# Kernel tuning notes

Hardware: AMD Instinct MI355X
Metric: run time of the kernel (lower is better)

Reference implementation:

```python
import jax, jax.numpy as jnp
import numpy as np

B, S, V, E, H = 256, 256, 32000, 1024, 1024


def setup_inputs() -> dict:
    key = jax.random.key(0)
    k0, k1, k2, k3 = jax.random.split(key, 4)
    inputs = jax.random.randint(k0, (B, S), 0, V, dtype=jnp.int32)
    emb = jax.random.normal(k1, (V, E), dtype=jnp.float32) * 0.02
    # Combined gate weights in flax LSTMCell gate order (i, f, g, o).
    # flax uses per-gate Dense layers; stacking them into [E,4H]/[H,4H] is equivalent.
    Wi = jax.random.normal(k2, (E, 4 * H), dtype=jnp.float32) * 0.02  # input->gates (no bias in flax dense_i)
    Wh = jax.random.normal(k3, (H, 4 * H), dtype=jnp.float32) * 0.02  # hidden->gates
    b = jnp.zeros((4 * H,), dtype=jnp.float32)  # bias lives on dense_h in flax
    return {"inputs": inputs, "emb": emb, "Wi": Wi, "Wh": Wh, "b": b}


def reference(inputs, emb, Wi, Wh, b):
    x = emb[inputs]  # [B,S,E] embedding lookup
    # Precompute all input projections at once (math-identical, one big GEMM).
    xW = jnp.einsum('bse,eg->bsg', x, Wi) + b  # [B,S,4H]

    def step(carry, xw_t):
        h, c = carry
        z = xw_t + h @ Wh  # [B,4H]
        i, f, g, o = jnp.split(z, 4, axis=-1)
        c = jax.nn.sigmoid(f) * c + jax.nn.sigmoid(i) * jnp.tanh(g)
        h = jax.nn.sigmoid(o) * jnp.tanh(c)
        return (h, c), h

    h0 = jnp.zeros((x.shape[0], Wh.shape[0]), dtype=x.dtype)
    (h, c), outs = jax.lax.scan(step, (h0, h0), jnp.swapaxes(xW, 0, 1))  # scan over time
    outputs = jnp.swapaxes(outs, 0, 1)  # [B,S,H]
    return outputs, h, c
```

## Files before the change

### kernel.cpp

```cpp
#include <hip/hip_runtime.h>
#include <hip/hip_bf16.h>
#include <stdint.h>


#define B_ 256
#define S_ 256
#define E_ 1024
#define H_ 1024
#define G_ 4096
#define M_ 65536

typedef float  f32x4  __attribute__((ext_vector_type(4)));
typedef __bf16 bf16x8 __attribute__((ext_vector_type(8)));

#define MFMA16(a, b, c) __builtin_amdgcn_mfma_f32_16x16x32_bf16((a), (b), (c), 0, 0, 0)

__device__ __forceinline__ void gload_lds16(const void* g, void* l) {
  __builtin_amdgcn_global_load_lds(
      (__attribute__((address_space(1))) void*)(g),
      (__attribute__((address_space(3))) void*)(l), 16, 0, 0);
}

__device__ __forceinline__ float sigm(float x) { return 1.f / (1.f + __expf(-x)); }
__device__ __forceinline__ float tanhfast(float x) {
  float e = __expf(-2.f * x);
  return (1.f - e) / (1.f + e);
}
__device__ __forceinline__ float bf_lo(unsigned v) { return __uint_as_float(v << 16); }
__device__ __forceinline__ float bf_hi(unsigned v) { return __uint_as_float(v & 0xffff0000u); }

__global__ __launch_bounds__(256) void zero_init(uint4* h16) {
  int i = blockIdx.x * 256 + threadIdx.x;
  uint4 z; z.x = z.y = z.z = z.w = 0u;
  if (i < 32768) h16[i] = z;
}
__global__ __launch_bounds__(256) void zero_flags(unsigned* flags) {
  flags[blockIdx.x * 256 + threadIdx.x] = 0u;
}

__global__ __launch_bounds__(256) void transpose_cast(const float* __restrict__ in,
                                                      __bf16* __restrict__ out) {
  __shared__ __bf16 tile[32][33];
  const int c0 = blockIdx.x * 32;
  const int r0 = blockIdx.y * 32;
  const int tx = threadIdx.x & 31, ty = threadIdx.x >> 5;
#pragma unroll
  for (int p = 0; p < 4; ++p) {
    const int rr = ty + p * 8;
    tile[rr][tx] = (__bf16)in[(size_t)(r0 + rr) * G_ + c0 + tx];
  }
  __syncthreads();
#pragma unroll
  for (int p = 0; p < 4; ++p) {
    const int rr = ty + p * 8;
    out[(size_t)(c0 + rr) * E_ + r0 + tx] = tile[tx][rr];
  }
}

union U16b { uint4 v; __bf16 h[8]; };
__global__ __launch_bounds__(256) void gather_cast(const int* __restrict__ idx,
                                                   const float* __restrict__ emb,
                                                   __bf16* __restrict__ X) {
  const size_t gid  = (size_t)blockIdx.x * 256 + threadIdx.x;
  const size_t base = gid * 8;
  const int r = (int)(base >> 10);
  const int e = (int)(base & 1023);
  const int row = idx[r];
  const float4* s = (const float4*)(emb + (size_t)row * E_ + e);
  const float4 v0 = s[0], v1 = s[1];
  U16b u;
  u.h[0] = (__bf16)v0.x; u.h[1] = (__bf16)v0.y; u.h[2] = (__bf16)v0.z; u.h[3] = (__bf16)v0.w;
  u.h[4] = (__bf16)v1.x; u.h[5] = (__bf16)v1.y; u.h[6] = (__bf16)v1.z; u.h[7] = (__bf16)v1.w;
  *(uint4*)(X + base) = u.v;
}

__global__ __launch_bounds__(256) void gemm_xw(const __bf16* __restrict__ X,
                                               const __bf16* __restrict__ WiT,
                                               const float* __restrict__ bias,
                                               __bf16* __restrict__ XW2) {
  __shared__ __bf16 As[128 * 32];
  __shared__ __bf16 Bs[128 * 32];
  __shared__ __bf16 eps[64][136];
  const int tid = threadIdx.x;
  const int lane = tid & 63;
  const int wid = tid >> 6;
  const int bn = blockIdx.x & 31;
  const int bm = blockIdx.x >> 5;
  const int row0 = bm * 128, col0 = bn * 128;
  const int wr = (wid >> 1) * 64, wc = (wid & 1) * 64;
  const int srow = tid >> 2, schunk = tid & 3;
  const char* gA = (const char*)(X + (size_t)(row0 + srow) * E_) + schunk * 16;
  const char* gB = (const char*)(WiT + (size_t)(col0 + srow) * E_) + schunk * 16;
  char* lA = (char*)As + wid * 1024;
  char* lB = (char*)Bs + wid * 1024;
  const int fr = lane & 15, kb = lane >> 4;

  f32x4 acc[4][4] = {};

  for (int kt = 0; kt < 32; ++kt) {
    gload_lds16(gA + kt * 64,              lA);
    gload_lds16(gA + kt * 64 + 64 * 2048,  lA + 4096);
    gload_lds16(gB + kt * 64,              lB);
    gload_lds16(gB + kt * 64 + 64 * 2048,  lB + 4096);
    __syncthreads();
    bf16x8 a[4], b[4];
#pragma unroll
    for (int m = 0; m < 4; ++m)
      a[m] = *(const bf16x8*)((const char*)As + (wr + m * 16 + fr) * 64 + kb * 16);
#pragma unroll
    for (int n = 0; n < 4; ++n)
      b[n] = *(const bf16x8*)((const char*)Bs + (wc + n * 16 + fr) * 64 + kb * 16);
#pragma unroll
    for (int m = 0; m < 4; ++m)
#pragma unroll
      for (int n = 0; n < 4; ++n)
        acc[m][n] = MFMA16(a[m], b[n], acc[m][n]);
    __syncthreads();
  }

  float bv[4];
#pragma unroll
  for (int n = 0; n < 4; ++n) bv[n] = bias[col0 + wc + n * 16 + fr];

  const int gate = col0 >> 10;
  const int cg0  = (col0 & 1023) >> 5;

#pragma unroll
  for (int h = 0; h < 2; ++h) {
    if ((wid >> 1) == h) {
#pragma unroll
      for (int m = 0; m < 4; ++m)
#pragma unroll
        for (int n = 0; n < 4; ++n)
#pragma unroll
          for (int r = 0; r < 4; ++r)
            eps[m * 16 + kb * 4 + r][wc + n * 16 + fr] = (__bf16)(acc[m][n][r] + bv[n]);
    }
    __syncthreads();
    {
      const int row = tid >> 2, ch = tid & 3;
      const int r_m = row0 + h * 64 + row;
      const uint4* s = (const uint4*)&eps[row][ch * 32];
      uint4* d = (uint4*)(XW2 + ((size_t)r_m * 32 + (cg0 + ch)) * 128 + gate * 32);
#pragma unroll
      for (int i = 0; i < 4; ++i) d[i] = s[i];
    }
    __syncthreads();
  }
}

__global__ __launch_bounds__(512, 2) void lstm_scan(
    const __bf16* __restrict__ WhT, const __bf16* __restrict__ XW2,
    __bf16* __restrict__ hb0, __bf16* __restrict__ hb1,
    float* __restrict__ outp, float* __restrict__ hfin,
    float* __restrict__ cfin, unsigned* __restrict__ flags) {
  __shared__ __bf16 As[32 * 1024];
  __shared__ float  zs[4][32][34];
  __shared__ int    sgrp[2];
  const int tid = threadIdx.x;
  const int lane = tid & 63;
  const int wid = tid >> 6;

  if (tid == 0) {
    unsigned xcd;
    asm volatile("s_getreg_b32 %0, hwreg(HW_REG_XCC_ID)" : "=s"(xcd));
    xcd &= 7u;
    unsigned slot = __hip_atomic_fetch_add(&flags[512 + xcd], 1u,
                                           __ATOMIC_RELAXED, __HIP_MEMORY_SCOPE_AGENT);
    sgrp[0] = (int)xcd;
    sgrp[1] = (int)(slot & 31u);
  }
  __syncthreads();
  const int bg = sgrp[0];
  const int cg = sgrp[1];
  const int b0 = bg * 32;
  const int c0 = cg * 32;
  unsigned* grpflags = flags + bg * 64;

  const int wg = wid & 3;
  const int nh = wid >> 2;
  const int fr = lane & 15, kb = lane >> 4;
  const __bf16* wb = WhT + (size_t)(wg * 1024 + c0 + nh * 16 + fr) * H_ + kb * 8;

  bf16x8 W[32];
#pragma unroll
  for (int j = 0; j < 32; ++j) W[j] = *(const bf16x8*)(wb + j * 32);

  const int crow = tid >> 4, ccolb = (tid & 15) * 2;
  const size_t sidx = (size_t)(b0 + crow) * H_ + c0 + ccolb;
  const __bf16* xwrow = XW2 + ((size_t)(b0 + crow) * S_ * 32 + cg) * 128 + ccolb;
  float creg0 = 0.f, creg1 = 0.f;

#pragma unroll 1
  for (int t = 0; t < S_; ++t) {
    const __bf16* hin = (t & 1) ? hb1 : hb0;
    __bf16* hout = (t & 1) ? hb0 : hb1;

    const __bf16* p = xwrow + (size_t)t * 4096;
    const unsigned xw0 = *(const unsigned*)(p);
    const unsigned xw1 = *(const unsigned*)(p + 32);
    const unsigned xw2 = *(const unsigned*)(p + 64);
    const unsigned xw3 = *(const unsigned*)(p + 96);

    if (t > 0) {
      if (tid < 32) {
        const unsigned tgt = (unsigned)t;
        while (__hip_atomic_load(&grpflags[tid], __ATOMIC_RELAXED,
                                 __HIP_MEMORY_SCOPE_AGENT) < tgt)
          __builtin_amdgcn_s_sleep(1);
      }
      __syncthreads();
    }

    {
      uint4 sv[8];
#pragma unroll
      for (int i = 0; i < 8; ++i) {
        const int ci = i * 512 + tid;
        const int row = ci >> 7, cch = ci & 127;
        const void* src = (const char*)(hin + (size_t)(b0 + row) * H_) + cch * 16;
        asm volatile("global_load_dwordx4 %0, %1, off sc0"
                     : "=&v"(sv[i]) : "v"(src) : "memory");
      }
      asm volatile("s_waitcnt vmcnt(0)" ::: "memory");
      __builtin_amdgcn_sched_barrier(0);
#pragma unroll
      for (int i = 0; i < 8; ++i) {
        const int ci = i * 512 + tid;
        const int row = ci >> 7, cch = ci & 127;
        *(uint4*)((char*)As + row * 2048 + ((cch ^ (row & 7)) * 16)) = sv[i];
      }
    }
    __syncthreads();

    f32x4 acc0 = {0.f, 0.f, 0.f, 0.f}, acc1 = {0.f, 0.f, 0.f, 0.f};
#pragma unroll
    for (int j = 0; j < 32; ++j) {
      const int ck = j * 4 + kb;
      bf16x8 alo = *(const bf16x8*)((const char*)As + fr * 2048 +
                                    ((ck ^ (fr & 7)) * 16));
      bf16x8 ahi = *(const bf16x8*)((const char*)As + (16 + fr) * 2048 +
                                    ((ck ^ (fr & 7)) * 16));
      acc0 = MFMA16(alo, W[j], acc0);
      acc1 = MFMA16(ahi, W[j], acc1);
    }
#pragma unroll
    for (int r = 0; r < 4; ++r) {
      zs[wg][kb * 4 + r][nh * 16 + fr]      = acc0[r];
      zs[wg][16 + kb * 4 + r][nh * 16 + fr] = acc1[r];
    }
    __syncthreads();

    const float2 zi2 = *(const float2*)&zs[0][crow][ccolb];
    const float2 zf2 = *(const float2*)&zs[1][crow][ccolb];
    const float2 zg2 = *(const float2*)&zs[2][crow][ccolb];
    const float2 zo2 = *(const float2*)&zs[3][crow][ccolb];
    const float zi0 = zi2.x + bf_lo(xw0), zi1 = zi2.y + bf_hi(xw0);
    const float zf0 = zf2.x + bf_lo(xw1), zf1 = zf2.y + bf_hi(xw1);
    const float zg0 = zg2.x + bf_lo(xw2), zg1 = zg2.y + bf_hi(xw2);
    const float zo0 = zo2.x + bf_lo(xw3), zo1 = zo2.y + bf_hi(xw3);
    const float cv0 = sigm(zf0) * creg0 + sigm(zi0) * tanhfast(zg0);
    const float cv1 = sigm(zf1) * creg1 + sigm(zi1) * tanhfast(zg1);
    creg0 = cv0; creg1 = cv1;
    const float hv0 = sigm(zo0) * tanhfast(cv0);
    const float hv1 = sigm(zo1) * tanhfast(cv1);

    union { __bf16 h[2]; unsigned u; } up;
    up.h[0] = (__bf16)hv0; up.h[1] = (__bf16)hv1;
    float2 o2; o2.x = hv0; o2.y = hv1;

    {
      void* dst = (void*)(hout + sidx);
      asm volatile("global_store_dword %0, %1, off sc0"
                   :: "v"(dst), "v"(up.u) : "memory");
    }

    if (t == S_ - 1) {
      *(float2*)(outp + ((size_t)(b0 + crow) * S_ + t) * H_ + c0 + ccolb) = o2;
      float2 c2; c2.x = cv0; c2.y = cv1;
      *(float2*)(hfin + sidx) = o2;
      *(float2*)(cfin + sidx) = c2;
    } else {
      asm volatile("s_waitcnt vmcnt(0)" ::: "memory");
      __builtin_amdgcn_s_barrier();
      if (tid == 0)
        __hip_atomic_store(&grpflags[cg], (unsigned)(t + 1),
                           __ATOMIC_RELAXED, __HIP_MEMORY_SCOPE_AGENT);
      *(float2*)(outp + ((size_t)(b0 + crow) * S_ + t) * H_ + c0 + ccolb) = o2;
    }
  }
}

extern "C" void kernel_launch(void* const* d_in, const int* in_sizes, int n_in,
                              void* d_out, int out_size, void* d_ws, size_t ws_size,
                              hipStream_t stream) {
  const int*   inp  = (const int*)d_in[0];
  const float* emb  = (const float*)d_in[1];
  const float* Wi   = (const float*)d_in[2];
  const float* Wh   = (const float*)d_in[3];
  const float* bias = (const float*)d_in[4];

  char* ws = (char*)d_ws;
  __bf16* WiT = (__bf16*)(ws);
  __bf16* WhT = (__bf16*)(ws + 8388608);
  __bf16* hb0 = (__bf16*)(ws + 16777216);
  __bf16* hb1 = (__bf16*)(ws + 17301504);
  __bf16* X   = (__bf16*)(ws + 17825792);
  __bf16* XW2 = (__bf16*)(ws + 152043520);
  unsigned* flags = (unsigned*)(ws + 17825792);

  float* outp = (float*)d_out;
  float* hfin = outp + (size_t)M_ * H_;
  float* cfin = hfin + (size_t)B_ * H_;

  zero_init<<<128, 256, 0, stream>>>((uint4*)hb0);
  transpose_cast<<<dim3(128, 32), 256, 0, stream>>>(Wi, WiT);
  transpose_cast<<<dim3(128, 32), 256, 0, stream>>>(Wh, WhT);
  gather_cast<<<32768, 256, 0, stream>>>(inp, emb, X);
  gemm_xw<<<16384, 256, 0, stream>>>(X, WiT, bias, XW2);
  zero_flags<<<4, 256, 0, stream>>>(flags);
  lstm_scan<<<256, 512, 0, stream>>>(WhT, XW2, hb0, hb1, outp, hfin, cfin, flags);
}
```

Baseline: 2.087 ms.

## Split recurrent GEMM across K halves instead of N halves per wave

Waves previously split the 32 output columns into two 16-column halves, each reducing over all of K. Now each wave computes all 32 columns over half of K and loads both 16-column weight tiles for its K half. Each A fragment read from LDS then feeds two MFMAs, halving the shared-memory reads per MFMA. The cost is a two-phase reduction through LDS (one half stores, the other adds) with an extra __syncthreads on every timestep of the serial recurrence.

```diff
diff --git a/kernel.cpp b/kernel.cpp
--- a/kernel.cpp
+++ b/kernel.cpp
@@ -178,13 +178,18 @@
   unsigned* grpflags = flags + bg * 64;
 
   const int wg = wid & 3;
-  const int nh = wid >> 2;
+  const int kh = wid >> 2;
   const int fr = lane & 15, kb = lane >> 4;
-  const __bf16* wb = WhT + (size_t)(wg * 1024 + c0 + nh * 16 + fr) * H_ + kb * 8;
-
-  bf16x8 W[32];
-#pragma unroll
-  for (int j = 0; j < 32; ++j) W[j] = *(const bf16x8*)(wb + j * 32);
+
+  bf16x8 W[2][16];
+  {
+    const __bf16* wbase = WhT + (size_t)(wg * 1024 + c0) * H_ + kh * 512 + kb * 8;
+#pragma unroll
+    for (int n = 0; n < 2; ++n)
+#pragma unroll
+      for (int j = 0; j < 16; ++j)
+        W[n][j] = *(const bf16x8*)(wbase + (size_t)(n * 16 + fr) * H_ + j * 32);
+  }
 
   const int crow = tid >> 4, ccolb = (tid & 15) * 2;
   const size_t sidx = (size_t)(b0 + crow) * H_ + c0 + ccolb;
@@ -233,21 +238,38 @@
     }
     __syncthreads();
 
-    f32x4 acc0 = {0.f, 0.f, 0.f, 0.f}, acc1 = {0.f, 0.f, 0.f, 0.f};
-#pragma unroll
-    for (int j = 0; j < 32; ++j) {
-      const int ck = j * 4 + kb;
+    f32x4 acc[2][2] = {};
+#pragma unroll
+    for (int j = 0; j < 16; ++j) {
+      const int ck = kh * 64 + j * 4 + kb;
       bf16x8 alo = *(const bf16x8*)((const char*)As + fr * 2048 +
                                     ((ck ^ (fr & 7)) * 16));
       bf16x8 ahi = *(const bf16x8*)((const char*)As + (16 + fr) * 2048 +
                                     ((ck ^ (fr & 7)) * 16));
-      acc0 = MFMA16(alo, W[j], acc0);
-      acc1 = MFMA16(ahi, W[j], acc1);
-    }
-#pragma unroll
-    for (int r = 0; r < 4; ++r) {
-      zs[wg][kb * 4 + r][nh * 16 + fr]      = acc0[r];
-      zs[wg][16 + kb * 4 + r][nh * 16 + fr] = acc1[r];
+      acc[0][0] = MFMA16(alo, W[0][j], acc[0][0]);
+      acc[0][1] = MFMA16(alo, W[1][j], acc[0][1]);
+      acc[1][0] = MFMA16(ahi, W[0][j], acc[1][0]);
+      acc[1][1] = MFMA16(ahi, W[1][j], acc[1][1]);
+    }
+
+    if (kh) {
+#pragma unroll
+      for (int rh = 0; rh < 2; ++rh)
+#pragma unroll
+        for (int n = 0; n < 2; ++n)
+#pragma unroll
+          for (int r = 0; r < 4; ++r)
+            zs[wg][rh * 16 + kb * 4 + r][n * 16 + fr] = acc[rh][n][r];
+    }
+    __syncthreads();
+    if (!kh) {
+#pragma unroll
+      for (int rh = 0; rh < 2; ++rh)
+#pragma unroll
+        for (int n = 0; n < 2; ++n)
+#pragma unroll
+          for (int r = 0; r < 4; ++r)
+            zs[wg][rh * 16 + kb * 4 + r][n * 16 + fr] += acc[rh][n][r];
     }
     __syncthreads();
 
```

Result: faster. 1.923 ms (-7.9%).

## Split-K recurrent GEMM across waves, loading h directly into registers

Applied to the files above, without the earlier changes.

The per-step recurrent GEMM changes from splitting the gate columns across waves to splitting the K dimension four ways. Each wave now keeps weights for all four gates over a quarter of K and loads its h slice straight from global memory into MFMA operands. This removes the LDS staging copy of h and one barrier per step. In exchange it adds a cross-wave reduction of partial sums through shared memory, and each wave now issues several small global loads per row instead of coalesced tile loads.

```diff
diff --git a/kernel.cpp b/kernel.cpp
--- a/kernel.cpp
+++ b/kernel.cpp
@@ -14,6 +14,10 @@
 typedef __bf16 bf16x8 __attribute__((ext_vector_type(8)));
 
 #define MFMA16(a, b, c) __builtin_amdgcn_mfma_f32_16x16x32_bf16((a), (b), (c), 0, 0, 0)
+
+#define ALOAD(dst, ptr, OFF)                                            \
+  asm volatile("global_load_dwordx4 %0, %1, off offset:" #OFF " sc0"    \
+               : "=&v"(dst) : "v"(ptr) : "memory")
 
 __device__ __forceinline__ void gload_lds16(const void* g, void* l) {
   __builtin_amdgcn_global_load_lds(
@@ -154,9 +158,9 @@
     __bf16* __restrict__ hb0, __bf16* __restrict__ hb1,
     float* __restrict__ outp, float* __restrict__ hfin,
     float* __restrict__ cfin, unsigned* __restrict__ flags) {
-  __shared__ __bf16 As[32 * 1024];
-  __shared__ float  zs[4][32][34];
-  __shared__ int    sgrp[2];
+  __shared__ float zsp[3][4][32][34];
+  __shared__ float zs[4][32][34];
+  __shared__ int   sgrp[2];
   const int tid = threadIdx.x;
   const int lane = tid & 63;
   const int wid = tid >> 6;
@@ -177,14 +181,19 @@
   const int c0 = cg * 32;
   unsigned* grpflags = flags + bg * 64;
 
-  const int wg = wid & 3;
-  const int nh = wid >> 2;
+  const int cs = wid & 1;
+  const int kq = wid >> 1;
   const int fr = lane & 15, kb = lane >> 4;
-  const __bf16* wb = WhT + (size_t)(wg * 1024 + c0 + nh * 16 + fr) * H_ + kb * 8;
-
-  bf16x8 W[32];
-#pragma unroll
-  for (int j = 0; j < 32; ++j) W[j] = *(const bf16x8*)(wb + j * 32);
+
+  bf16x8 W[4][8];
+#pragma unroll
+  for (int g = 0; g < 4; ++g) {
+    const __bf16* wbase = WhT + (size_t)(g * 1024 + c0 + cs * 16 + fr) * H_ +
+                          kq * 256 + kb * 8;
+#pragma unroll
+    for (int ks = 0; ks < 8; ++ks)
+      W[g][ks] = *(const bf16x8*)(wbase + ks * 32);
+  }
 
   const int crow = tid >> 4, ccolb = (tid & 15) * 2;
   const size_t sidx = (size_t)(b0 + crow) * H_ + c0 + ccolb;
@@ -212,42 +221,55 @@
       __syncthreads();
     }
 
+    f32x4 acc[2][4] = {};
     {
-      uint4 sv[8];
-#pragma unroll
-      for (int i = 0; i < 8; ++i) {
-        const int ci = i * 512 + tid;
-        const int row = ci >> 7, cch = ci & 127;
-        const void* src = (const char*)(hin + (size_t)(b0 + row) * H_) + cch * 16;
-        asm volatile("global_load_dwordx4 %0, %1, off sc0"
-                     : "=&v"(sv[i]) : "v"(src) : "memory");
+      const __bf16* a0p = hin + (size_t)(b0 + fr) * H_ + kq * 256 + kb * 8;
+#pragma unroll
+      for (int rt = 0; rt < 2; ++rt) {
+        const __bf16* ap = a0p + (size_t)rt * 16 * H_;
+        uint4 sv[8];
+        ALOAD(sv[0], ap, 0);
+        ALOAD(sv[1], ap, 64);
+        ALOAD(sv[2], ap, 128);
+        ALOAD(sv[3], ap, 192);
+        ALOAD(sv[4], ap, 256);
+        ALOAD(sv[5], ap, 320);
+        ALOAD(sv[6], ap, 384);
+        ALOAD(sv[7], ap, 448);
+        asm volatile("s_waitcnt vmcnt(0)" ::: "memory");
+        __builtin_amdgcn_sched_barrier(0);
+#pragma unroll
+        for (int ks = 0; ks < 8; ++ks) {
+          const bf16x8 av = *(const bf16x8*)&sv[ks];
+#pragma unroll
+          for (int g = 0; g < 4; ++g)
+            acc[rt][g] = MFMA16(av, W[g][ks], acc[rt][g]);
+        }
       }
-      asm volatile("s_waitcnt vmcnt(0)" ::: "memory");
-      __builtin_amdgcn_sched_barrier(0);
-#pragma unroll
-      for (int i = 0; i < 8; ++i) {
-        const int ci = i * 512 + tid;
-        const int row = ci >> 7, cch = ci & 127;
-        *(uint4*)((char*)As + row * 2048 + ((cch ^ (row & 7)) * 16)) = sv[i];
-      }
-    }
-    __syncthreads();
-
-    f32x4 acc0 = {0.f, 0.f, 0.f, 0.f}, acc1 = {0.f, 0.f, 0.f, 0.f};
-#pragma unroll
-    for (int j = 0; j < 32; ++j) {
-      const int ck = j * 4 + kb;
-      bf16x8 alo = *(const bf16x8*)((const char*)As + fr * 2048 +
-                                    ((ck ^ (fr & 7)) * 16));
-      bf16x8 ahi = *(const bf16x8*)((const char*)As + (16 + fr) * 2048 +
-                                    ((ck ^ (fr & 7)) * 16));
-      acc0 = MFMA16(alo, W[j], acc0);
-      acc1 = MFMA16(ahi, W[j], acc1);
-    }
-#pragma unroll
-    for (int r = 0; r < 4; ++r) {
-      zs[wg][kb * 4 + r][nh * 16 + fr]      = acc0[r];
-      zs[wg][16 + kb * 4 + r][nh * 16 + fr] = acc1[r];
+    }
+
+    if (kq > 0) {
+#pragma unroll
+      for (int rt = 0; rt < 2; ++rt)
+#pragma unroll
+        for (int g = 0; g < 4; ++g)
+#pragma unroll
+          for (int r = 0; r < 4; ++r)
+            zsp[kq - 1][g][rt * 16 + kb * 4 + r][cs * 16 + fr] = acc[rt][g][r];
+    }
+    __syncthreads();
+    if (kq == 0) {
+#pragma unroll
+      for (int rt = 0; rt < 2; ++rt)
+#pragma unroll
+        for (int g = 0; g < 4; ++g)
+#pragma unroll
+          for (int r = 0; r < 4; ++r) {
+            const int row = rt * 16 + kb * 4 + r;
+            const int col = cs * 16 + fr;
+            zs[g][row][col] = acc[rt][g][r] + zsp[0][g][row][col] +
+                              zsp[1][g][row][col] + zsp[2][g][row][col];
+          }
     }
     __syncthreads();
 
```

Result: slower. 2.587 ms (+24.0%).
